# Performance work log

Measured on AMD Instinct MI355X. Metric: run time of the kernel, lower is better.

## Reference

```python
import jax
jax.config.update("jax_enable_x64", True)  # Sinkhorn runs in f64, matching torch's d.double()
import jax.numpy as jnp
import numpy as np

N, D, K = 32768, 128, 1024
TAU = 0.2
SK_EPS = 0.005
SK_ITERS = 3


def setup_inputs() -> dict:
    key = jax.random.key(0)
    k1, k2 = jax.random.split(key)
    x = jax.random.normal(k1, (N, D), dtype=jnp.float32)
    codebook = jax.random.normal(k2, (K, D), dtype=jnp.float32) * 0.02  # embedding.weight
    return {"x": x, "codebook": codebook}


def _l2norm(v):
    # F.normalize with eps=1e-12
    n = jnp.linalg.norm(v, axis=-1, keepdims=True)
    return v / jnp.maximum(n, 1e-12)


def _center_distance(d):
    d = jnp.where(jnp.isnan(d), jnp.zeros_like(d), d)
    mx, mn = d.max(), d.min()
    middle = (mx + mn) / 2
    amplitude = jnp.maximum(mx - middle + 1e-5, 1e-5)
    return (d - middle) / amplitude


def _sinkhorn(d, epsilon, iters):
    # d: [N, K] in f64; Q: [K, N]
    Q = jnp.exp(-d / epsilon).T
    Kc, B = Q.shape
    Q = Q / jnp.maximum(Q.sum(), 1e-5)

    def body(Q, _):
        Q = Q / Q.sum(axis=1, keepdims=True) / Kc
        Q = Q / Q.sum(axis=0, keepdims=True) / B
        return Q, None

    Q, _ = jax.lax.scan(body, Q, None, length=iters)
    return (Q * B).T  # [N, K]


def reference(x, codebook):
    latent = x.reshape(-1, codebook.shape[-1])  # [N, D]
    cos_sim = _l2norm(latent) @ _l2norm(codebook).T  # [N, K]
    d = (1.0 - cos_sim) / TAU

    # training path with sk_epsilon > 0: center + Sinkhorn (no_grad in torch)
    dc = _center_distance(jax.lax.stop_gradient(d))
    Q = _sinkhorn(dc.astype(jnp.float64), SK_EPS, SK_ITERS)
    indices = jnp.argmax(Q, axis=-1)  # [N]

    x_q = codebook[indices].reshape(x.shape)

    # cross-entropy(cos_sim / tau, indices.detach())
    logits = cos_sim / TAU
    logp = jax.nn.log_softmax(logits, axis=-1)
    loss = -jnp.mean(jnp.take_along_axis(logp, indices[:, None], axis=-1))

    # straight-through estimator
    x_q = x + jax.lax.stop_gradient(x_q - x)
    return x_q, loss, indices
```

## Files before the change

### kernel.cpp

```cpp
#include <hip/hip_runtime.h>
#include <cstddef>

#define NPTS 32768
#define DDIM 128
#define KCB  1024

typedef __attribute__((ext_vector_type(8))) short short8;
typedef __attribute__((ext_vector_type(4))) float f32x4;


__device__ __forceinline__ float hw_exp2(float x) {
#if __has_builtin(__builtin_amdgcn_exp2f)
  return __builtin_amdgcn_exp2f(x);
#else
  return exp2f(x);
#endif
}

__device__ __forceinline__ void atomic_add_f64(double* p, double v) {
  __hip_atomic_fetch_add(p, v, __ATOMIC_RELAXED, __HIP_MEMORY_SCOPE_AGENT);
}

__device__ __forceinline__ unsigned short bf16_rne(float v) {
  unsigned u = __float_as_uint(v);
  unsigned r = u + 0x7FFFu + ((u >> 16) & 1u);
  return (unsigned short)(r >> 16);
}
__device__ __forceinline__ float bf16_tof(unsigned short h) {
  return __uint_as_float((unsigned)h << 16);
}

__device__ __forceinline__ float div_mark(float x, float c, float rc) {
  float q0 = x * rc;
  float r  = fmaf(-c, q0, x);
  return fmaf(r, rc, q0);
}

__device__ __forceinline__ double sweep_E(float cv, float middle, float amp, float rc_amp) {
  float d  = div_mark(1.0f - cv, 0.2f, 1.0f / 0.2f);
  float dc = div_mark(d - middle, amp, rc_amp);
  double xl2 = (double)dc * (-288.53900817779268);
  double kd  = rint(xl2);
  float  fr  = (float)(xl2 - kd);
  float  m   = hw_exp2(fr);
  long long bits = ((long long)(1023 + (int)kd)) << 52;
  return (double)m * __longlong_as_double(bits);
}

__device__ __forceinline__ double score_exponent(float cv, float middle, float amplitude) {
  float d  = (1.0f - cv) / 0.2f;
  float dc = (d - middle) / amplitude;
  return (double)dc * (-(1.0 / 0.005));
}

__device__ __forceinline__ unsigned enc_f32(float f) {
  unsigned u = __float_as_uint(f);
  return (u & 0x80000000u) ? ~u : (u | 0x80000000u);
}
__device__ __forceinline__ float dec_f32(unsigned e) {
  unsigned u = (e & 0x80000000u) ? (e & 0x7FFFFFFFu) : ~e;
  return __uint_as_float(u);
}

#if __has_builtin(__builtin_amdgcn_global_load_lds)
#define HAVE_ASYNC_LDS 1
typedef __attribute__((address_space(3))) unsigned int lds_u32_t;
typedef const __attribute__((address_space(1))) unsigned int glb_u32_t;
__device__ __forceinline__ void async_ld16(const void* g, void* l) {
  __builtin_amdgcn_global_load_lds((glb_u32_t*)g, (lds_u32_t*)l, 16, 0, 0);
}
#else
#define HAVE_ASYNC_LDS 0
#endif


__global__ __launch_bounds__(1024) void vq_init_kernel(double* __restrict__ u123,
                                                       double* __restrict__ loss_part,
                                                       unsigned* __restrict__ maxenc,
                                                       unsigned* __restrict__ minenc) {
  int t = threadIdx.x;
  for (int i = t; i < 3 * KCB; i += 1024) u123[i] = 0.0;
  loss_part[t] = 0.0;
  if (t == 0) {
    *maxenc = 0u;
    *minenc = 0xFFFFFFFFu;
  }
}

__global__ __launch_bounds__(128) void vq_normalize_rows(const float* __restrict__ in,
                                                         float* __restrict__ out) {
  int row = blockIdx.x;
  int t = threadIdx.x;
  float v = in[(size_t)row * DDIM + t];
  float s = v * v;
#pragma unroll
  for (int off = 32; off; off >>= 1) s += __shfl_down(s, off, 64);
  __shared__ float red[2];
  if ((t & 63) == 0) red[t >> 6] = s;
  __syncthreads();
  float norm = sqrtf(red[0] + red[1]);
  out[(size_t)row * DDIM + t] = v / fmaxf(norm, 1e-12f);
}

__global__ __launch_bounds__(128) void vq_normalize_split(const float* __restrict__ in,
                                                          unsigned short* __restrict__ oh,
                                                          unsigned short* __restrict__ ol) {
  int row = blockIdx.x;
  int t = threadIdx.x;
  float v = in[(size_t)row * DDIM + t];
  float s = v * v;
#pragma unroll
  for (int off = 32; off; off >>= 1) s += __shfl_down(s, off, 64);
  __shared__ float red[2];
  if ((t & 63) == 0) red[t >> 6] = s;
  __syncthreads();
  float norm = sqrtf(red[0] + red[1]);
  float xnv = v / fmaxf(norm, 1e-12f);
  unsigned short h = bf16_rne(xnv);
  float fh = bf16_tof(h);
  unsigned short l = bf16_rne(xnv - fh);
  size_t idx = (size_t)row * DDIM + t;
  oh[idx] = h;
  ol[idx] = l;
}

#define LROWS 32

__global__ __launch_bounds__(256) void vq_gemm_mfma(const unsigned short* __restrict__ Ah,
                                                    const unsigned short* __restrict__ Al,
                                                    const unsigned short* __restrict__ Bh,
                                                    const unsigned short* __restrict__ Bl,
                                                    float* __restrict__ Cm,
                                                    unsigned* __restrict__ maxenc,
                                                    unsigned* __restrict__ minenc) {
  __shared__ unsigned short Ahs[128 * LROWS], Als[128 * LROWS];
  __shared__ unsigned short Bhs[128 * LROWS], Bls[128 * LROWS];
  __shared__ float redmx[4], redmn[4];
  int tid = threadIdx.x;
  int lane = tid & 63, wv = tid >> 6;
  int wr = wv >> 1, wc = wv & 1;
  int n0 = blockIdx.x * 128;
  int c0 = blockIdx.y * 128;
  int fr = lane & 15;
  int kq = (lane >> 4) * 8;
  f32x4 acc[4][4] = {};

#pragma unroll 1
  for (int ks = 0; ks < 4; ++ks) {
    int kc = ks * 32;
#pragma unroll
    for (int l = 0; l < 2; ++l) {
      int idx = tid + l * 256;
      int row = idx >> 2;
      int sub = idx & 3;
      size_t ga = (size_t)(n0 + row) * DDIM + kc + sub * 8;
      size_t gb = (size_t)(c0 + row) * DDIM + kc + sub * 8;
#if HAVE_ASYNC_LDS
      int wbase = (l * 256 + wv * 64) * 8;
      async_ld16(Ah + ga, Ahs + wbase);
      async_ld16(Al + ga, Als + wbase);
      async_ld16(Bh + gb, Bhs + wbase);
      async_ld16(Bl + gb, Bls + wbase);
#else
      int lo = idx * 8;
      *(short8*)&Ahs[lo] = *(const short8*)(Ah + ga);
      *(short8*)&Als[lo] = *(const short8*)(Al + ga);
      *(short8*)&Bhs[lo] = *(const short8*)(Bh + gb);
      *(short8*)&Bls[lo] = *(const short8*)(Bl + gb);
#endif
    }
    __syncthreads();
    short8 ah[4], al[4], bh[4], bl[4];
#pragma unroll
    for (int rt = 0; rt < 4; ++rt) {
      int lo = (wr * 64 + rt * 16 + fr) * LROWS + kq;
      ah[rt] = *(const short8*)&Ahs[lo];
      al[rt] = *(const short8*)&Als[lo];
    }
#pragma unroll
    for (int ct = 0; ct < 4; ++ct) {
      int lo = (wc * 64 + ct * 16 + fr) * LROWS + kq;
      bh[ct] = *(const short8*)&Bhs[lo];
      bl[ct] = *(const short8*)&Bls[lo];
    }
#pragma unroll
    for (int rt = 0; rt < 4; ++rt) {
#pragma unroll
      for (int ct = 0; ct < 4; ++ct) {
        acc[rt][ct] = __builtin_amdgcn_mfma_f32_16x16x32_bf16(ah[rt], bh[ct], acc[rt][ct], 0, 0, 0);
        acc[rt][ct] = __builtin_amdgcn_mfma_f32_16x16x32_bf16(ah[rt], bl[ct], acc[rt][ct], 0, 0, 0);
        acc[rt][ct] = __builtin_amdgcn_mfma_f32_16x16x32_bf16(al[rt], bh[ct], acc[rt][ct], 0, 0, 0);
        acc[rt][ct] = __builtin_amdgcn_mfma_f32_16x16x32_bf16(al[rt], bl[ct], acc[rt][ct], 0, 0, 0);
      }
    }
    __syncthreads();
  }

  float mx = -3.402823466e38f, mn = 3.402823466e38f;
  int orow = (lane >> 4) * 4, ocol = lane & 15;
  int rn0 = n0 + wr * 64, rc0 = c0 + wc * 64;
#pragma unroll
  for (int rt = 0; rt < 4; ++rt) {
#pragma unroll
    for (int ct = 0; ct < 4; ++ct) {
#pragma unroll
      for (int r = 0; r < 4; ++r) {
        float v = acc[rt][ct][r];
        mx = fmaxf(mx, v);
        mn = fminf(mn, v);
        Cm[(size_t)(rn0 + rt * 16 + orow + r) * KCB + (rc0 + ct * 16 + ocol)] = v;
      }
    }
  }
#pragma unroll
  for (int off = 32; off; off >>= 1) {
    mx = fmaxf(mx, __shfl_down(mx, off, 64));
    mn = fminf(mn, __shfl_down(mn, off, 64));
  }
  if (lane == 0) { redmx[wv] = mx; redmn[wv] = mn; }
  __syncthreads();
  if (tid == 0) {
    mx = fmaxf(fmaxf(redmx[0], redmx[1]), fmaxf(redmx[2], redmx[3]));
    mn = fminf(fminf(redmn[0], redmn[1]), fminf(redmn[2], redmn[3]));
    atomicMax(maxenc, enc_f32(mx));
    atomicMin(minenc, enc_f32(mn));
  }
}

__global__ void vq_scalarize(const unsigned* __restrict__ maxenc,
                             const unsigned* __restrict__ minenc,
                             float* __restrict__ scal) {
  float cosmax = dec_f32(*maxenc);
  float cosmin = dec_f32(*minenc);
  float mx_d = (1.0f - cosmin) / 0.2f;
  float mn_d = (1.0f - cosmax) / 0.2f;
  float middle = (mx_d + mn_d) / 2.0f;
  float amplitude = fmaxf(mx_d - middle + 1e-5f, 1e-5f);
  scal[0] = middle;
  scal[1] = amplitude;
  scal[2] = 1.0f / amplitude;
}

#define SROWS 32
#define SRPW  8

__global__ __launch_bounds__(256) void vq_sweep(const float* __restrict__ Cm,
                                                const float* __restrict__ scal,
                                                const double* __restrict__ Rvec,
                                                const double* __restrict__ alpha_p,
                                                double* __restrict__ u_out) {
  int t = threadIdx.x;
  int lane = t & 63, wv = t >> 6;
  int n0 = blockIdx.x * SROWS + wv * SRPW;
  float middle = scal[0], amp = scal[1], rc = scal[2];
  bool hasR = (Rvec != nullptr);
  double Rreg[16];
  double ainv = 0.0;
  if (hasR) {
#pragma unroll
    for (int c = 0; c < 4; ++c)
#pragma unroll
      for (int e = 0; e < 4; ++e) Rreg[c * 4 + e] = Rvec[c * 256 + lane * 4 + e];
    ainv = alpha_p[0] * 32768.0;
  }
  double up[16] = {};
  float4 cva[4], cvb[4];
  {
    const float4* row0 = (const float4*)(Cm + (size_t)n0 * KCB);
#pragma unroll
    for (int c = 0; c < 4; ++c) cva[c] = row0[c * 64 + lane];
  }
#pragma unroll 1
  for (int r = 0; r < SRPW; ++r) {
    int rn = (r < SRPW - 1) ? r + 1 : r;
    const float4* rown = (const float4*)(Cm + (size_t)(n0 + rn) * KCB);
#pragma unroll
    for (int c = 0; c < 4; ++c) cvb[c] = rown[c * 64 + lane];
    double e[16];
#pragma unroll
    for (int c = 0; c < 4; ++c) {
      e[c * 4 + 0] = sweep_E(cva[c].x, middle, amp, rc);
      e[c * 4 + 1] = sweep_E(cva[c].y, middle, amp, rc);
      e[c * 4 + 2] = sweep_E(cva[c].z, middle, amp, rc);
      e[c * 4 + 3] = sweep_E(cva[c].w, middle, amp, rc);
    }
    if (hasR) {
      double s = 0.0;
#pragma unroll
      for (int i = 0; i < 16; ++i) s += e[i] * Rreg[i];
#pragma unroll
      for (int off = 1; off < 64; off <<= 1) s += __shfl_xor(s, off, 64);
      double C = 1.0 / (ainv * s);
#pragma unroll
      for (int i = 0; i < 16; ++i) up[i] += e[i] * C;
    } else {
#pragma unroll
      for (int i = 0; i < 16; ++i) up[i] += e[i];
    }
#pragma unroll
    for (int c = 0; c < 4; ++c) cva[c] = cvb[c];
  }
  __shared__ double su[4][KCB];
#pragma unroll
  for (int c = 0; c < 4; ++c)
#pragma unroll
    for (int e = 0; e < 4; ++e) su[wv][c * 256 + lane * 4 + e] = up[c * 4 + e];
  __syncthreads();
#pragma unroll
  for (int j = 0; j < 4; ++j) {
    int k = (t + ((blockIdx.x + j) & 3) * 256) & (KCB - 1);
    double v = su[0][k] + su[1][k] + su[2][k] + su[3][k];
    atomic_add_f64(&u_out[k], v);
  }
}

__global__ __launch_bounds__(1024) void vq_finalize_u(const double* __restrict__ u,
                                                      double* __restrict__ alpha_p,
                                                      double* __restrict__ R,
                                                      double* __restrict__ lnR,
                                                      int mode) {
  int k = threadIdx.x;
  double uk = u[k];
  __shared__ double red[16];
  __shared__ double s_alpha;
  if (mode == 0) {
    double s = uk;
#pragma unroll
    for (int off = 32; off; off >>= 1) s += __shfl_down(s, off, 64);
    if ((k & 63) == 0) red[k >> 6] = s;
    __syncthreads();
    if (k == 0) {
      double s0 = 0.0;
      for (int w = 0; w < 16; ++w) s0 += red[w];
      double a = 1.0 / fmax(s0, 1e-5);
      s_alpha = a;
      alpha_p[0] = a;
    }
    __syncthreads();
  }
  double alpha = (mode == 0) ? s_alpha : alpha_p[0];
  double r = 1.0 / (alpha * 1024.0 * uk);
  R[k] = r;
  if (mode == 2) lnR[k] = log(r);
}

#define FRPW 4
#define MARGIN 0.08f
#define LOG2E 1.44269504088896340736f

__global__ __launch_bounds__(256) void vq_final_pass(const float* __restrict__ Cm,
                                                     const float* __restrict__ x,
                                                     const float* __restrict__ cb,
                                                     const float* __restrict__ xn,
                                                     const float* __restrict__ cn,
                                                     const double* __restrict__ lnR,
                                                     const float* __restrict__ scal,
                                                     double* __restrict__ loss_part,
                                                     float* __restrict__ out_xq,
                                                     float* __restrict__ out_idx) {
  int t = threadIdx.x;
  int lane = t & 63, wv = t >> 6;
  int n0 = blockIdx.x * (4 * FRPW) + wv * FRPW;
  float middle = scal[0], amplitude = scal[1], rc_amp = scal[2];
  float lnRf[16];
  double lnRd[16];
#pragma unroll
  for (int c = 0; c < 4; ++c)
#pragma unroll
    for (int e = 0; e < 4; ++e) {
      double v = lnR[c * 256 + lane * 4 + e];
      lnRd[c * 4 + e] = v;
      lnRf[c * 4 + e] = (float)v;
    }

  double loss_loc = 0.0;
  float4 cva[4], cvb[4];
  {
    const float4* row0 = (const float4*)(Cm + (size_t)n0 * KCB);
#pragma unroll
    for (int c = 0; c < 4; ++c) cva[c] = row0[c * 64 + lane];
  }
#pragma unroll 1
  for (int r = 0; r < FRPW; ++r) {
    int n = n0 + r;
    int rn = (r < FRPW - 1) ? r + 1 : r;
    const float4* rown = (const float4*)(Cm + (size_t)(n0 + rn) * KCB);
#pragma unroll
    for (int c = 0; c < 4; ++c) cvb[c] = rown[c * 64 + lane];

    float lv[16];
    float sv[16];
    float b1 = -3.402823466e38f, b2 = -3.402823466e38f;
    int k1 = 0;
    float lmax = -3.402823466e38f;
#pragma unroll
    for (int c = 0; c < 4; ++c) {
#pragma unroll
      for (int e = 0; e < 4; ++e) {
        float cvv = (e == 0) ? cva[c].x : (e == 1) ? cva[c].y : (e == 2) ? cva[c].z : cva[c].w;
        int k = c * 256 + lane * 4 + e;
        float d  = div_mark(1.0f - cvv, 0.2f, 5.0f);
        float dc = div_mark(d - middle, amplitude, rc_amp);
        float s  = fmaf(dc, -200.0f, lnRf[c * 4 + e]);
        sv[c * 4 + e] = s;
        if (s > b1) { b2 = b1; b1 = s; k1 = k; }
        else if (s > b2) b2 = s;
        float l = div_mark(cvv, 0.2f, 5.0f);
        lv[c * 4 + e] = l;
        lmax = fmaxf(lmax, l);
      }
    }
#pragma unroll
    for (int off = 1; off < 64; off <<= 1) {
      float o1 = __shfl_xor(b1, off, 64);
      int ok = __shfl_xor(k1, off, 64);
      float o2 = __shfl_xor(b2, off, 64);
      float om = __shfl_xor(lmax, off, 64);
      float cand2;
      if (o1 > b1 || (o1 == b1 && ok < k1)) { cand2 = fmaxf(b1, o2); b1 = o1; k1 = ok; }
      else cand2 = fmaxf(o1, o2);
      b2 = fmaxf(b2, cand2);
      lmax = fmaxf(lmax, om);
    }
    int bestk = k1;
    if (b1 - b2 < MARGIN) {
      double pbest = -1.0e308;
      int pk = KCB;
      const float* xr = xn + (size_t)n * DDIM;
      float thr = b1 - MARGIN;
#pragma unroll 1
      for (int i = 0; i < 16; ++i) {
        if (sv[i] >= thr) {
          int k = (i >> 2) * 256 + lane * 4 + (i & 3);
          const float* cr = cn + (size_t)k * DDIM;
          float dot = 0.0f;
          for (int d = 0; d < DDIM; ++d) dot = fmaf(xr[d], cr[d], dot);
          double ps = score_exponent(dot, middle, amplitude) + lnRd[i];
          if (ps > pbest || (ps == pbest && k < pk)) { pbest = ps; pk = k; }
        }
      }
#pragma unroll
      for (int off = 1; off < 64; off <<= 1) {
        double ob = __shfl_xor(pbest, off, 64);
        int ok = __shfl_xor(pk, off, 64);
        if (ob > pbest || (ob == pbest && ok < pk)) { pbest = ob; pk = ok; }
      }
      bestk = pk;
    }
    float se = 0.0f;
    float lb = 0.0f;
#pragma unroll
    for (int c = 0; c < 4; ++c) {
#pragma unroll
      for (int e = 0; e < 4; ++e) {
        int k = c * 256 + lane * 4 + e;
        se += hw_exp2((lv[c * 4 + e] - lmax) * LOG2E);
        if (k == bestk) lb = lv[c * 4 + e];
      }
    }
#pragma unroll
    for (int off = 1; off < 64; off <<= 1) {
      se += __shfl_xor(se, off, 64);
      lb += __shfl_xor(lb, off, 64);
    }
    loss_loc += (double)(-(lb - lmax - logf(se)));
    if (lane == 0) out_idx[n] = (float)bestk;
    float2 xv = *(const float2*)&x[(size_t)n * DDIM + lane * 2];
    float2 cbv = *(const float2*)&cb[(size_t)bestk * DDIM + lane * 2];
    float2 o;
    o.x = xv.x + (cbv.x - xv.x);
    o.y = xv.y + (cbv.y - xv.y);
    *(float2*)&out_xq[(size_t)n * DDIM + lane * 2] = o;
#pragma unroll
    for (int c = 0; c < 4; ++c) cva[c] = cvb[c];
  }
  if (lane == 0) atomic_add_f64(&loss_part[(blockIdx.x * 4 + wv) & (KCB - 1)], loss_loc);
}

__global__ __launch_bounds__(1024) void vq_loss_div(const double* __restrict__ lp,
                                                    float* __restrict__ out_loss) {
  int t = threadIdx.x;
  double s = lp[t];
#pragma unroll
  for (int off = 32; off; off >>= 1) s += __shfl_down(s, off, 64);
  __shared__ double red[16];
  if ((t & 63) == 0) red[t >> 6] = s;
  __syncthreads();
  if (t == 0) {
    double tot = 0.0;
    for (int w = 0; w < 16; ++w) tot += red[w];
    out_loss[0] = (float)(tot / 32768.0);
  }
}


extern "C" void kernel_launch(void* const* d_in, const int* in_sizes, int n_in,
                              void* d_out, int out_size, void* d_ws, size_t ws_size,
                              hipStream_t stream) {
  const float* x  = (const float*)d_in[0];
  const float* cb = (const float*)d_in[1];
  float* out = (float*)d_out;
  float* out_xq   = out;
  float* out_loss = out + (size_t)NPTS * DDIM;
  float* out_idx  = out + (size_t)NPTS * DDIM + 1;

  char* w = (char*)d_ws;
  unsigned short* xh = (unsigned short*)w;
  unsigned short* xl = xh + (size_t)NPTS * DDIM;
  unsigned short* ch = xl + (size_t)NPTS * DDIM;
  unsigned short* cl = ch + (size_t)KCB * DDIM;
  float* xn = (float*)w;
  float* cn = xn + (size_t)NPTS * DDIM;
  float* cosm = (float*)(w + (size_t)16896 * 1024);
  double* u1  = (double*)(cosm + (size_t)NPTS * KCB);
  double* u2  = u1 + KCB;
  double* u3  = u2 + KCB;
  double* R   = u3 + KCB;
  double* lnR = R + KCB;
  double* loss_part = lnR + KCB;
  double* alpha_p   = loss_part + KCB;
  unsigned* maxenc = (unsigned*)(alpha_p + 1);
  unsigned* minenc = maxenc + 1;
  float* scal = (float*)(minenc + 1);

  vq_init_kernel<<<1, 1024, 0, stream>>>(u1, loss_part, maxenc, minenc);

  vq_normalize_split<<<NPTS, 128, 0, stream>>>(x, xh, xl);
  vq_normalize_split<<<KCB, 128, 0, stream>>>(cb, ch, cl);
  vq_gemm_mfma<<<dim3(NPTS / 128, KCB / 128), 256, 0, stream>>>(xh, xl, ch, cl, cosm,
                                                                maxenc, minenc);

  vq_normalize_rows<<<NPTS, 128, 0, stream>>>(x, xn);
  vq_normalize_rows<<<KCB, 128, 0, stream>>>(cb, cn);
  vq_scalarize<<<1, 1, 0, stream>>>(maxenc, minenc, scal);

  vq_sweep<<<NPTS / SROWS, 256, 0, stream>>>(cosm, scal, nullptr, alpha_p, u1);
  vq_finalize_u<<<1, 1024, 0, stream>>>(u1, alpha_p, R, lnR, 0);
  vq_sweep<<<NPTS / SROWS, 256, 0, stream>>>(cosm, scal, R, alpha_p, u2);
  vq_finalize_u<<<1, 1024, 0, stream>>>(u2, alpha_p, R, lnR, 1);
  vq_sweep<<<NPTS / SROWS, 256, 0, stream>>>(cosm, scal, R, alpha_p, u3);
  vq_finalize_u<<<1, 1024, 0, stream>>>(u3, alpha_p, R, lnR, 2);

  vq_final_pass<<<NPTS / (4 * FRPW), 256, 0, stream>>>(cosm, x, cb, xn, cn, lnR, scal,
                                                       loss_part, out_xq, out_idx);
  vq_loss_div<<<1, 1024, 0, stream>>>(loss_part, out_loss);
}
```

Before: 322.1 us.

## Double-buffer GEMM LDS tiles and prefetch two rows ahead in sweeps

The MFMA GEMM now keeps two LDS buffers and issues the global-to-LDS load for the next K-slice right after reading fragments for the current one, so the load overlaps the MFMAs; its K loop is also fully unrolled. The Sinkhorn sweep and final-argmax kernels switch from one-row-ahead prefetch to a two-slot register ring that loads the row two steps ahead, to hide more global-memory latency. The cost is double the GEMM LDS footprint, which can lower occupancy. In the row kernels, indexing buf[slot] with a runtime slot inside a non-unrolled loop may spill to scratch or add selects.

```diff
diff --git a/kernel.cpp b/kernel.cpp
--- a/kernel.cpp
+++ b/kernel.cpp
@@ -133,8 +133,8 @@
                                                     float* __restrict__ Cm,
                                                     unsigned* __restrict__ maxenc,
                                                     unsigned* __restrict__ minenc) {
-  __shared__ unsigned short Ahs[128 * LROWS], Als[128 * LROWS];
-  __shared__ unsigned short Bhs[128 * LROWS], Bls[128 * LROWS];
+  __shared__ unsigned short Ahs[2][128 * LROWS], Als[2][128 * LROWS];
+  __shared__ unsigned short Bhs[2][128 * LROWS], Bls[2][128 * LROWS];
   __shared__ float redmx[4], redmn[4];
   int tid = threadIdx.x;
   int lane = tid & 63, wv = tid >> 6;
@@ -145,8 +145,7 @@
   int kq = (lane >> 4) * 8;
   f32x4 acc[4][4] = {};
 
-#pragma unroll 1
-  for (int ks = 0; ks < 4; ++ks) {
+  auto stage = [&](int ks, int b) {
     int kc = ks * 32;
 #pragma unroll
     for (int l = 0; l < 2; ++l) {
@@ -157,32 +156,40 @@
       size_t gb = (size_t)(c0 + row) * DDIM + kc + sub * 8;
 #if HAVE_ASYNC_LDS
       int wbase = (l * 256 + wv * 64) * 8;
-      async_ld16(Ah + ga, Ahs + wbase);
-      async_ld16(Al + ga, Als + wbase);
-      async_ld16(Bh + gb, Bhs + wbase);
-      async_ld16(Bl + gb, Bls + wbase);
+      async_ld16(Ah + ga, &Ahs[b][wbase]);
+      async_ld16(Al + ga, &Als[b][wbase]);
+      async_ld16(Bh + gb, &Bhs[b][wbase]);
+      async_ld16(Bl + gb, &Bls[b][wbase]);
 #else
       int lo = idx * 8;
-      *(short8*)&Ahs[lo] = *(const short8*)(Ah + ga);
-      *(short8*)&Als[lo] = *(const short8*)(Al + ga);
-      *(short8*)&Bhs[lo] = *(const short8*)(Bh + gb);
-      *(short8*)&Bls[lo] = *(const short8*)(Bl + gb);
+      *(short8*)&Ahs[b][lo] = *(const short8*)(Ah + ga);
+      *(short8*)&Als[b][lo] = *(const short8*)(Al + ga);
+      *(short8*)&Bhs[b][lo] = *(const short8*)(Bh + gb);
+      *(short8*)&Bls[b][lo] = *(const short8*)(Bl + gb);
 #endif
     }
-    __syncthreads();
+  };
+
+  stage(0, 0);
+  __syncthreads();
+
+#pragma unroll
+  for (int ks = 0; ks < 4; ++ks) {
+    int cur = ks & 1;
     short8 ah[4], al[4], bh[4], bl[4];
 #pragma unroll
     for (int rt = 0; rt < 4; ++rt) {
       int lo = (wr * 64 + rt * 16 + fr) * LROWS + kq;
-      ah[rt] = *(const short8*)&Ahs[lo];
-      al[rt] = *(const short8*)&Als[lo];
+      ah[rt] = *(const short8*)&Ahs[cur][lo];
+      al[rt] = *(const short8*)&Als[cur][lo];
     }
 #pragma unroll
     for (int ct = 0; ct < 4; ++ct) {
       int lo = (wc * 64 + ct * 16 + fr) * LROWS + kq;
-      bh[ct] = *(const short8*)&Bhs[lo];
-      bl[ct] = *(const short8*)&Bls[lo];
-    }
+      bh[ct] = *(const short8*)&Bhs[cur][lo];
+      bl[ct] = *(const short8*)&Bls[cur][lo];
+    }
+    if (ks < 3) stage(ks + 1, cur ^ 1);
 #pragma unroll
     for (int rt = 0; rt < 4; ++rt) {
 #pragma unroll
@@ -264,25 +271,29 @@
     ainv = alpha_p[0] * 32768.0;
   }
   double up[16] = {};
-  float4 cva[4], cvb[4];
+  float4 buf[2][4];
   {
-    const float4* row0 = (const float4*)(Cm + (size_t)n0 * KCB);
-#pragma unroll
-    for (int c = 0; c < 4; ++c) cva[c] = row0[c * 64 + lane];
+    const float4* r0 = (const float4*)(Cm + (size_t)n0 * KCB);
+    const float4* r1 = (const float4*)(Cm + (size_t)(n0 + 1) * KCB);
+#pragma unroll
+    for (int c = 0; c < 4; ++c) { buf[0][c] = r0[c * 64 + lane]; buf[1][c] = r1[c * 64 + lane]; }
   }
 #pragma unroll 1
   for (int r = 0; r < SRPW; ++r) {
-    int rn = (r < SRPW - 1) ? r + 1 : r;
-    const float4* rown = (const float4*)(Cm + (size_t)(n0 + rn) * KCB);
-#pragma unroll
-    for (int c = 0; c < 4; ++c) cvb[c] = rown[c * 64 + lane];
+    int slot = r & 1;
     double e[16];
 #pragma unroll
     for (int c = 0; c < 4; ++c) {
-      e[c * 4 + 0] = sweep_E(cva[c].x, middle, amp, rc);
-      e[c * 4 + 1] = sweep_E(cva[c].y, middle, amp, rc);
-      e[c * 4 + 2] = sweep_E(cva[c].z, middle, amp, rc);
-      e[c * 4 + 3] = sweep_E(cva[c].w, middle, amp, rc);
+      e[c * 4 + 0] = sweep_E(buf[slot][c].x, middle, amp, rc);
+      e[c * 4 + 1] = sweep_E(buf[slot][c].y, middle, amp, rc);
+      e[c * 4 + 2] = sweep_E(buf[slot][c].z, middle, amp, rc);
+      e[c * 4 + 3] = sweep_E(buf[slot][c].w, middle, amp, rc);
+    }
+    {
+      int rn = (r + 2 < SRPW) ? r + 2 : SRPW - 1;
+      const float4* rown = (const float4*)(Cm + (size_t)(n0 + rn) * KCB);
+#pragma unroll
+      for (int c = 0; c < 4; ++c) buf[slot][c] = rown[c * 64 + lane];
     }
     if (hasR) {
       double s = 0.0;
@@ -297,8 +308,6 @@
 #pragma unroll
       for (int i = 0; i < 16; ++i) up[i] += e[i];
     }
-#pragma unroll
-    for (int c = 0; c < 4; ++c) cva[c] = cvb[c];
   }
   __shared__ double su[4][KCB];
 #pragma unroll
@@ -374,19 +383,26 @@
     }
 
   double loss_loc = 0.0;
-  float4 cva[4], cvb[4];
+  float4 buf[2][4];
   {
-    const float4* row0 = (const float4*)(Cm + (size_t)n0 * KCB);
-#pragma unroll
-    for (int c = 0; c < 4; ++c) cva[c] = row0[c * 64 + lane];
+    const float4* r0 = (const float4*)(Cm + (size_t)n0 * KCB);
+    const float4* r1 = (const float4*)(Cm + (size_t)(n0 + 1) * KCB);
+#pragma unroll
+    for (int c = 0; c < 4; ++c) { buf[0][c] = r0[c * 64 + lane]; buf[1][c] = r1[c * 64 + lane]; }
   }
 #pragma unroll 1
   for (int r = 0; r < FRPW; ++r) {
     int n = n0 + r;
-    int rn = (r < FRPW - 1) ? r + 1 : r;
-    const float4* rown = (const float4*)(Cm + (size_t)(n0 + rn) * KCB);
-#pragma unroll
-    for (int c = 0; c < 4; ++c) cvb[c] = rown[c * 64 + lane];
+    int slot = r & 1;
+    float4 cva[4];
+#pragma unroll
+    for (int c = 0; c < 4; ++c) cva[c] = buf[slot][c];
+    {
+      int rn = (r + 2 < FRPW) ? r + 2 : FRPW - 1;
+      const float4* rown = (const float4*)(Cm + (size_t)(n0 + rn) * KCB);
+#pragma unroll
+      for (int c = 0; c < 4; ++c) buf[slot][c] = rown[c * 64 + lane];
+    }
 
     float lv[16];
     float sv[16];
@@ -471,8 +487,6 @@
     o.x = xv.x + (cbv.x - xv.x);
     o.y = xv.y + (cbv.y - xv.y);
     *(float2*)&out_xq[(size_t)n * DDIM + lane * 2] = o;
-#pragma unroll
-    for (int c = 0; c < 4; ++c) cva[c] = cvb[c];
   }
   if (lane == 0) atomic_add_f64(&loss_part[(blockIdx.x * 4 + wv) & (KCB - 1)], loss_loc);
 }
```

New measurement: 494.9 us. 1.54x slower.

## Double-buffer LDS tiles in the MFMA GEMM to overlap loads with compute

Applied to the files above, without the earlier changes.

Splits the shared-memory A/B hi/lo tiles into two buffers and issues the global-to-LDS load for the next K slice before running the MFMAs on the current one. The loop is fully unrolled and starts with one prologue stage. The goal is to hide global load latency behind the matrix math. The cost is double the LDS footprint (about 64KB), which may lower occupancy. The rest of the loop body, including where the barriers sit, is not fully visible.

```diff
diff --git a/kernel.cpp b/kernel.cpp
--- a/kernel.cpp
+++ b/kernel.cpp
@@ -133,8 +133,8 @@
                                                     float* __restrict__ Cm,
                                                     unsigned* __restrict__ maxenc,
                                                     unsigned* __restrict__ minenc) {
-  __shared__ unsigned short Ahs[128 * LROWS], Als[128 * LROWS];
-  __shared__ unsigned short Bhs[128 * LROWS], Bls[128 * LROWS];
+  __shared__ unsigned short Ahs[2][128 * LROWS], Als[2][128 * LROWS];
+  __shared__ unsigned short Bhs[2][128 * LROWS], Bls[2][128 * LROWS];
   __shared__ float redmx[4], redmn[4];
   int tid = threadIdx.x;
   int lane = tid & 63, wv = tid >> 6;
@@ -145,8 +145,7 @@
   int kq = (lane >> 4) * 8;
   f32x4 acc[4][4] = {};
 
-#pragma unroll 1
-  for (int ks = 0; ks < 4; ++ks) {
+  auto stage = [&](int ks, int b) {
     int kc = ks * 32;
 #pragma unroll
     for (int l = 0; l < 2; ++l) {
@@ -157,32 +156,40 @@
       size_t gb = (size_t)(c0 + row) * DDIM + kc + sub * 8;
 #if HAVE_ASYNC_LDS
       int wbase = (l * 256 + wv * 64) * 8;
-      async_ld16(Ah + ga, Ahs + wbase);
-      async_ld16(Al + ga, Als + wbase);
-      async_ld16(Bh + gb, Bhs + wbase);
-      async_ld16(Bl + gb, Bls + wbase);
+      async_ld16(Ah + ga, &Ahs[b][wbase]);
+      async_ld16(Al + ga, &Als[b][wbase]);
+      async_ld16(Bh + gb, &Bhs[b][wbase]);
+      async_ld16(Bl + gb, &Bls[b][wbase]);
 #else
       int lo = idx * 8;
-      *(short8*)&Ahs[lo] = *(const short8*)(Ah + ga);
-      *(short8*)&Als[lo] = *(const short8*)(Al + ga);
-      *(short8*)&Bhs[lo] = *(const short8*)(Bh + gb);
-      *(short8*)&Bls[lo] = *(const short8*)(Bl + gb);
+      *(short8*)&Ahs[b][lo] = *(const short8*)(Ah + ga);
+      *(short8*)&Als[b][lo] = *(const short8*)(Al + ga);
+      *(short8*)&Bhs[b][lo] = *(const short8*)(Bh + gb);
+      *(short8*)&Bls[b][lo] = *(const short8*)(Bl + gb);
 #endif
     }
-    __syncthreads();
+  };
+
+  stage(0, 0);
+  __syncthreads();
+
+#pragma unroll
+  for (int ks = 0; ks < 4; ++ks) {
+    int cur = ks & 1;
     short8 ah[4], al[4], bh[4], bl[4];
 #pragma unroll
     for (int rt = 0; rt < 4; ++rt) {
       int lo = (wr * 64 + rt * 16 + fr) * LROWS + kq;
-      ah[rt] = *(const short8*)&Ahs[lo];
-      al[rt] = *(const short8*)&Als[lo];
+      ah[rt] = *(const short8*)&Ahs[cur][lo];
+      al[rt] = *(const short8*)&Als[cur][lo];
     }
 #pragma unroll
     for (int ct = 0; ct < 4; ++ct) {
       int lo = (wc * 64 + ct * 16 + fr) * LROWS + kq;
-      bh[ct] = *(const short8*)&Bhs[lo];
-      bl[ct] = *(const short8*)&Bls[lo];
-    }
+      bh[ct] = *(const short8*)&Bhs[cur][lo];
+      bl[ct] = *(const short8*)&Bls[cur][lo];
+    }
+    if (ks < 3) stage(ks + 1, cur ^ 1);
 #pragma unroll
     for (int rt = 0; rt < 4; ++rt) {
 #pragma unroll
```

Result: no change. 318.9 us (-1.0%).
